# Optimization experiments

Measured on AMD Instinct MI355X. Metric: run time of the kernel, lower is better.

## Reference

```python
import jax, jax.numpy as jnp
import numpy as np

H = 4096; NH = 32; HD = 128; SCALE = HD ** -0.5
PREFILLS = [1024, 512, 768, 256]; DOFF = sum(PREFILLS)
DEC = 32; LMAX = 512; T = DOFF + DEC
NLORA = 4; RANK = 16
SEG = [0, 648, 1296, 1944, 2592]  # static lora segment offsets (cumsum of lens)
NEG = -1e30


def _rope_tables(pos):
    # pos: int array [...]; returns cos/sin of shape [..., HD]
    inv = 1.0 / (10000.0 ** (jnp.arange(0, HD, 2, dtype=jnp.float32) / HD))
    freqs = pos.astype(jnp.float32)[..., None] * inv
    emb = jnp.concatenate([freqs, freqs], axis=-1)
    return jnp.cos(emb), jnp.sin(emb)


def _apply_rope(x, cos, sin):
    # x: [..., HD]; cos/sin broadcastable to x
    x1, x2 = x[..., :HD // 2], x[..., HD // 2:]
    return x * cos + jnp.concatenate([-x2, x1], axis=-1) * sin


def _add_lora(y, x, wa, wb):
    # Punica add_lora: per-segment y += (x @ wa[i]) @ wb[i], segments static
    for i in range(NLORA):
        s, e = SEG[i], SEG[i + 1]
        y = y.at[s:e].add((x[s:e] @ wa[i]) @ wb[i])
    return y


def setup_inputs() -> dict:
    key = jax.random.key(0)
    ks = jax.random.split(key, 16)
    sc = np.float32(1.0 / np.sqrt(H))
    lsc = np.float32(1.0 / np.sqrt(H))
    inp = {
        "hidden_states": jax.random.normal(ks[0], (T, H), jnp.float32),
        "wq": jax.random.normal(ks[1], (H, H), jnp.float32) * sc,
        "wk": jax.random.normal(ks[2], (H, H), jnp.float32) * sc,
        "wv": jax.random.normal(ks[3], (H, H), jnp.float32) * sc,
        "wo": jax.random.normal(ks[4], (H, H), jnp.float32) * sc,
        "la_q": jax.random.normal(ks[5], (NLORA, H, RANK), jnp.float32) * lsc,
        "lb_q": jax.random.normal(ks[6], (NLORA, RANK, H), jnp.float32) * lsc,
        "la_k": jax.random.normal(ks[7], (NLORA, H, RANK), jnp.float32) * lsc,
        "lb_k": jax.random.normal(ks[8], (NLORA, RANK, H), jnp.float32) * lsc,
        "la_v": jax.random.normal(ks[9], (NLORA, H, RANK), jnp.float32) * lsc,
        "lb_v": jax.random.normal(ks[10], (NLORA, RANK, H), jnp.float32) * lsc,
        "la_o": jax.random.normal(ks[11], (NLORA, H, RANK), jnp.float32) * lsc,
        "lb_o": jax.random.normal(ks[12], (NLORA, RANK, H), jnp.float32) * lsc,
        "k_cache": jax.random.normal(ks[13], (DEC, LMAX, NH, HD), jnp.float32),
        "v_cache": jax.random.normal(ks[14], (DEC, LMAX, NH, HD), jnp.float32),
        "kv_lens": jax.random.randint(ks[15], (DEC,), 0, 450, jnp.int32),
    }
    return inp


def reference(hidden_states, wq, wk, wv, wo, la_q, lb_q, la_k, lb_k,
              la_v, lb_v, la_o, lb_o, k_cache, v_cache, kv_lens):
    # fused QKV + segmented batched LoRA
    q = _add_lora(hidden_states @ wq, hidden_states, la_q, lb_q)
    k = _add_lora(hidden_states @ wk, hidden_states, la_k, lb_k)
    v = _add_lora(hidden_states @ wv, hidden_states, la_v, lb_v)

    outs = []
    # ragged prefill: per-request causal attention with inline rotary (beg=0)
    off = 0
    for s_len in PREFILLS:
        qi = q[off:off + s_len].reshape(s_len, NH, HD)
        ki = k[off:off + s_len].reshape(s_len, NH, HD)
        vi = v[off:off + s_len].reshape(s_len, NH, HD)
        cos, sin = _rope_tables(jnp.arange(s_len))
        cos, sin = cos[:, None, :], sin[:, None, :]
        qi = _apply_rope(qi, cos, sin)
        ki = _apply_rope(ki, cos, sin)
        scores = jnp.einsum('qhd,khd->hqk', qi, ki) * SCALE
        causal = jnp.tril(jnp.ones((s_len, s_len), bool))
        scores = jnp.where(causal[None], scores, NEG)
        p = jax.nn.softmax(scores, axis=-1)
        outs.append(jnp.einsum('hqk,khd->qhd', p, vi).reshape(s_len, H))
        off += s_len

    # paged/batched decode: append new k/v at kv_lens, rope-on-the-fly attention
    qd = q[DOFF:].reshape(DEC, NH, HD)
    kd = k[DOFF:].reshape(DEC, NH, HD)
    vd = v[DOFF:].reshape(DEC, NH, HD)
    b = jnp.arange(DEC)
    kc = k_cache.at[b, kv_lens].set(kd)
    vc = v_cache.at[b, kv_lens].set(vd)
    cosq, sinq = _rope_tables(kv_lens)            # new token position = kv_len
    qd = _apply_rope(qd, cosq[:, None, :], sinq[:, None, :])
    cosk, sink = _rope_tables(jnp.arange(LMAX))   # cache positions 0..LMAX-1
    kc_r = _apply_rope(kc, cosk[None, :, None, :], sink[None, :, None, :])
    scores = jnp.einsum('bhd,blhd->bhl', qd, kc_r) * SCALE
    valid = jnp.arange(LMAX)[None, :] <= kv_lens[:, None]  # [DEC, LMAX]
    scores = jnp.where(valid[:, None, :], scores, NEG)
    p = jax.nn.softmax(scores, axis=-1)
    outs.append(jnp.einsum('bhl,blhd->bhd', p, vc).reshape(DEC, H))

    attn = jnp.concatenate(outs, axis=0)          # [T, H]
    o = attn @ wo
    o = _add_lora(o, attn, la_o, lb_o)
    return o
```

## Files before the change

### kernel.cpp

```cpp
#include <hip/hip_runtime.h>
#include <hip/hip_bf16.h>


#define H_    4096
#define NH_   32
#define HD_   128
#define T_    2592
#define DOFF_ 2560
#define DEC_  32
#define LMAX_ 512
#define RANK_ 16
#define MPAD_ 2816

__constant__ float SCALE_ = 0.08838834764831845f;

typedef __bf16 bf16x8 __attribute__((ext_vector_type(8)));
typedef __bf16 bf16x4 __attribute__((ext_vector_type(4)));
typedef float  f32x4  __attribute__((ext_vector_type(4)));

__device__ __forceinline__ void async_cp16(const __bf16* g, __bf16* l) {
    __builtin_amdgcn_global_load_lds(
        (const __attribute__((address_space(1))) void*)g,
        (__attribute__((address_space(3))) void*)l, 16, 0, 0);
}

__global__ __launch_bounds__(256)
void prep1_kernel(const float* __restrict__ X, __bf16* __restrict__ Xb,
                  const float* __restrict__ la0, const float* __restrict__ la1,
                  const float* __restrict__ la2, __bf16* __restrict__ TMP16,
                  const float* __restrict__ wq, const float* __restrict__ wk,
                  const float* __restrict__ wv, const float* __restrict__ wo,
                  __bf16* __restrict__ wT, __bf16* __restrict__ woT,
                  const float* __restrict__ lbq, const float* __restrict__ lbk,
                  const float* __restrict__ lbv, const float* __restrict__ lbo,
                  __bf16* __restrict__ WB16, __bf16* __restrict__ WBo16,
                  float* __restrict__ cost, float* __restrict__ sint)
{
    const int bid = blockIdx.x;
    const int tid = threadIdx.x;

    if (bid < T_) {
        const int r = bid;
        const float* xr = X + (size_t)r * H_;
        __bf16* br = Xb + (size_t)r * H_;
        #pragma unroll
        for (int i = 0; i < 4; ++i) {
            float4 v = ((const float4*)xr)[tid + i * 256];
            bf16x4 w; w[0] = (__bf16)v.x; w[1] = (__bf16)v.y; w[2] = (__bf16)v.z; w[3] = (__bf16)v.w;
            ((bf16x4*)br)[tid + i * 256] = w;
        }
        const int si = (r < 648) ? 0 : (r < 1296 ? 1 : (r < 1944 ? 2 : 3));
        const int c    = tid & 15;
        const int part = tid >> 4;
        const float* wa0 = la0 + (size_t)si * H_ * RANK_;
        const float* wa1 = la1 + (size_t)si * H_ * RANK_;
        const float* wa2 = la2 + (size_t)si * H_ * RANK_;
        float s0 = 0.f, s1 = 0.f, s2 = 0.f;
        const int h0 = part * 256;
        for (int h = h0; h < h0 + 256; ++h) {
            const float xv = xr[h];
            s0 += xv * wa0[(size_t)h * RANK_ + c];
            s1 += xv * wa1[(size_t)h * RANK_ + c];
            s2 += xv * wa2[(size_t)h * RANK_ + c];
        }
        __shared__ float red[3][16][17];
        red[0][part][c] = s0; red[1][part][c] = s1; red[2][part][c] = s2;
        __syncthreads();
        if (tid < 192) {
            const int z = tid >> 6, cc = tid & 63;
            float t = 0.f;
            if ((cc >> 4) == si) {
                #pragma unroll
                for (int p = 0; p < 16; ++p) t += red[z][p][cc & 15];
            }
            TMP16[((size_t)z * MPAD_ + r) * 64 + cc] = (__bf16)t;
        }
    } else if (bid < T_ + 16384) {
        const int t = bid - T_;
        const int z = t >> 12;
        const int rem = t & 4095;
        const int bx = (rem >> 6) * 64;
        const int by = (rem & 63) * 64;
        const float* W = (z == 0) ? wq : (z == 1 ? wk : (z == 2 ? wv : wo));
        __bf16* To = (z < 3) ? wT + (size_t)z * H_ * H_ : woT;
        __shared__ float s[64][65];
        #pragma unroll
        for (int i = 0; i < 4; ++i) {
            const int idx = i * 256 + tid;
            const int r  = idx >> 4;
            const int c4 = (idx & 15) * 4;
            float4 v = *(const float4*)&W[(size_t)(by + r) * H_ + bx + c4];
            s[r][c4] = v.x; s[r][c4 + 1] = v.y; s[r][c4 + 2] = v.z; s[r][c4 + 3] = v.w;
        }
        __syncthreads();
        #pragma unroll
        for (int i = 0; i < 2; ++i) {
            const int idx = i * 256 + tid;
            const int n  = idx >> 3;
            const int kc = (idx & 7) * 8;
            bf16x8 w;
            #pragma unroll
            for (int j = 0; j < 8; ++j) w[j] = (__bf16)s[kc + j][n];
            *(bf16x8*)&To[(size_t)(bx + n) * H_ + by + kc] = w;
        }
    } else if (bid < T_ + 16384 + 64) {
        const int t = bid - (T_ + 16384);
        const int z = t >> 4;
        const int n = (t & 15) * 256 + tid;
        const float* lb = (z == 0) ? lbq : (z == 1 ? lbk : (z == 2 ? lbv : lbo));
        __bf16* dst = (z < 3) ? WB16 + ((size_t)z * H_ + n) * 64 : WBo16 + (size_t)n * 64;
        __bf16 row[64];
        #pragma unroll
        for (int si = 0; si < 4; ++si)
            #pragma unroll
            for (int c = 0; c < 16; ++c)
                row[si * 16 + c] = (__bf16)lb[((size_t)si * 16 + c) * H_ + n];
        #pragma unroll
        for (int i = 0; i < 8; ++i) *(bf16x8*)&dst[i * 8] = *(const bf16x8*)&row[i * 8];
    } else {
        const int t = bid - (T_ + 16384 + 64);
        const int p = t * 4 + (tid >> 6);
        const int i = tid & 63;
        const float inv = powf(10000.f, -(float)(2 * i) / (float)HD_);
        const float a = (float)p * inv;
        cost[p * 64 + i] = cosf(a);
        sint[p * 64 + i] = sinf(a);
    }
}

__global__ __launch_bounds__(512, 2)
void gemm_qkv(const __bf16* __restrict__ A, const __bf16* __restrict__ Bt,
              const __bf16* __restrict__ TMP16, const __bf16* __restrict__ WB16,
              __bf16* __restrict__ O0, __bf16* __restrict__ O1, __bf16* __restrict__ O2, int M)
{
    const int hw = blockIdx.y * 21 + blockIdx.x;
    const int work = (hw & 7) * 126 + (hw >> 3);
    const int bm0 = (work % 21) * 128;
    const int bn0 = (work / 21) * 256;

    __shared__ __align__(16) __bf16 Asl[3][128 * 64];
    __shared__ __align__(16) __bf16 Bsl[3][256 * 64];

    const int tid = threadIdx.x, lane = tid & 63, wid = tid >> 6;
    const int wr = wid >> 2, wc = wid & 3;
    const int fr = lane & 15, fq = lane >> 4;

    int arow[2], aoff[2], brow[4], boff[4];
    #pragma unroll
    for (int i = 0; i < 2; ++i) {
        const int ci = i * 512 + tid;
        arow[i] = ci >> 3;
        aoff[i] = ((ci & 7) ^ (arow[i] & 7)) * 8;
    }
    #pragma unroll
    for (int i = 0; i < 4; ++i) {
        const int ci = i * 512 + tid;
        brow[i] = ci >> 3;
        boff[i] = ((ci & 7) ^ (brow[i] & 7)) * 8;
    }
    const __bf16* Ab = A  + (size_t)bm0 * H_;
    const __bf16* Bb = Bt + (size_t)bn0 * H_;

    auto stageA = [&](int buf, int kt2) {
        const int kb = kt2 * 64;
        #pragma unroll
        for (int i = 0; i < 2; ++i)
            async_cp16(Ab + (size_t)arow[i] * H_ + kb + aoff[i],
                       &Asl[buf][(i * 512 + wid * 64) * 8]);
    };
    auto stageB1 = [&](int buf, int kt2) {
        async_cp16(Bb + (size_t)brow[0] * H_ + kt2 * 64 + boff[0],
                   &Bsl[buf][(wid * 64) * 8]);
    };
    auto stageB3 = [&](int buf, int kt2) {
        const int kb = kt2 * 64;
        #pragma unroll
        for (int i = 1; i < 4; ++i)
            async_cp16(Bb + (size_t)brow[i] * H_ + kb + boff[i],
                       &Bsl[buf][(i * 512 + wid * 64) * 8]);
    };
    auto rdA = [&](int buf, int kh, int mi) -> bf16x8 {
        const int row = wr * 64 + mi * 16 + fr;
        const int pc  = (kh * 4 + fq) ^ (row & 7);
        return *(const bf16x8*)&Asl[buf][row * 64 + pc * 8];
    };
    auto rdB = [&](int buf, int kh, int nj) -> bf16x8 {
        const int row = wc * 64 + nj * 16 + fr;
        const int pc  = (kh * 4 + fq) ^ (row & 7);
        return *(const bf16x8*)&Bsl[buf][row * 64 + pc * 8];
    };

    f32x4 acc[4][4] = {};

    stageA(0, 0); stageB1(0, 0); stageB3(0, 0);
    stageA(1, 1); stageB1(1, 1); stageB3(1, 1);
    asm volatile("s_waitcnt vmcnt(6)");
    __builtin_amdgcn_sched_barrier(0);
    __builtin_amdgcn_s_barrier();

    const int NT = H_ / 64;
    int cur = 0, nxt = 2;
    for (int kt = 0; kt < NT; ++kt) {
        const bool pf = (kt + 2 < NT);
        bf16x8 af[4], bfr[4];

        #pragma unroll
        for (int mi = 0; mi < 4; ++mi) af[mi] = rdA(cur, 0, mi);
        #pragma unroll
        for (int nj = 0; nj < 4; ++nj) bfr[nj] = rdB(cur, 0, nj);
        if (pf) { stageA(nxt, kt + 2); stageB1(nxt, kt + 2); }
        __builtin_amdgcn_s_barrier();
        asm volatile("s_waitcnt lgkmcnt(0)");
        __builtin_amdgcn_sched_barrier(0);
        __builtin_amdgcn_s_setprio(1);
        #pragma unroll
        for (int mi = 0; mi < 4; ++mi)
            #pragma unroll
            for (int nj = 0; nj < 4; ++nj)
                acc[mi][nj] = __builtin_amdgcn_mfma_f32_16x16x32_bf16(af[mi], bfr[nj], acc[mi][nj], 0, 0, 0);
        __builtin_amdgcn_s_setprio(0);
        __builtin_amdgcn_s_barrier();

        #pragma unroll
        for (int mi = 0; mi < 4; ++mi) af[mi] = rdA(cur, 1, mi);
        #pragma unroll
        for (int nj = 0; nj < 4; ++nj) bfr[nj] = rdB(cur, 1, nj);
        if (pf) stageB3(nxt, kt + 2);
        __builtin_amdgcn_s_barrier();
        asm volatile("s_waitcnt lgkmcnt(0)");
        __builtin_amdgcn_sched_barrier(0);
        __builtin_amdgcn_s_setprio(1);
        #pragma unroll
        for (int mi = 0; mi < 4; ++mi)
            #pragma unroll
            for (int nj = 0; nj < 4; ++nj)
                acc[mi][nj] = __builtin_amdgcn_mfma_f32_16x16x32_bf16(af[mi], bfr[nj], acc[mi][nj], 0, 0, 0);
        __builtin_amdgcn_s_setprio(0);
        if (pf)               asm volatile("s_waitcnt vmcnt(6)");
        else if (kt + 1 < NT) asm volatile("s_waitcnt vmcnt(0)");
        __builtin_amdgcn_sched_barrier(0);
        __builtin_amdgcn_s_barrier();

        cur = (cur == 2) ? 0 : cur + 1;
        nxt = (nxt == 2) ? 0 : nxt + 1;
    }

    const int colbase = bn0 + wc * 64;
    const int mat = colbase >> 12;
    __bf16* O = (mat == 0) ? O0 : (mat == 1 ? O1 : O2);
    const __bf16* TPm = TMP16 + (size_t)mat * MPAD_ * 64;
    bf16x8 aT[4][2], bW[4][2];
    #pragma unroll
    for (int mi = 0; mi < 4; ++mi)
        #pragma unroll
        for (int kh = 0; kh < 2; ++kh)
            aT[mi][kh] = *(const bf16x8*)&TPm[(size_t)(bm0 + wr * 64 + mi * 16 + fr) * 64 + kh * 32 + fq * 8];
    #pragma unroll
    for (int nj = 0; nj < 4; ++nj)
        #pragma unroll
        for (int kh = 0; kh < 2; ++kh)
            bW[nj][kh] = *(const bf16x8*)&WB16[(size_t)(colbase + nj * 16 + fr) * 64 + kh * 32 + fq * 8];
    #pragma unroll
    for (int mi = 0; mi < 4; ++mi)
        #pragma unroll
        for (int nj = 0; nj < 4; ++nj) {
            acc[mi][nj] = __builtin_amdgcn_mfma_f32_16x16x32_bf16(aT[mi][0], bW[nj][0], acc[mi][nj], 0, 0, 0);
            acc[mi][nj] = __builtin_amdgcn_mfma_f32_16x16x32_bf16(aT[mi][1], bW[nj][1], acc[mi][nj], 0, 0, 0);
        }
    #pragma unroll
    for (int mi = 0; mi < 4; ++mi)
        #pragma unroll
        for (int nj = 0; nj < 4; ++nj) {
            const int cc = (colbase + nj * 16 + fr) & 4095;
            #pragma unroll
            for (int rr = 0; rr < 4; ++rr) {
                const int row = bm0 + wr * 64 + mi * 16 + fq * 4 + rr;
                if (row < M) O[(size_t)row * H_ + cc] = (__bf16)acc[mi][nj][rr];
            }
        }
}

__global__ __launch_bounds__(512, 2)
void gemm_out(const __bf16* __restrict__ A, const __bf16* __restrict__ Bt,
              const __bf16* __restrict__ TMPo16, const __bf16* __restrict__ WBo16,
              float* __restrict__ C, int M, int Ntot)
{
    const int NY = gridDim.y;
    const int total = gridDim.x * NY;
    const int bid = blockIdx.x * NY + blockIdx.y;
    const int q = total >> 3, r8 = total & 7;
    const int xcd = bid & 7, j = bid >> 3;
    const int swz = (xcd < r8 ? xcd * (q + 1) : r8 * (q + 1) + (xcd - r8) * q) + j;
    const int bm0 = (swz / NY) * 256;
    const int bn0 = (swz % NY) * 192;

    __shared__ __align__(16) __bf16 Asl[2][256 * 64];
    __shared__ __align__(16) __bf16 Bsl[2][192 * 64];

    const int tid = threadIdx.x, lane = tid & 63, wid = tid >> 6;
    const int wr = wid >> 2, wc = wid & 3;
    const int fr = lane & 15, fq = lane >> 4;

    int arow[4], aoff[4], brow[3], boff[3];
    #pragma unroll
    for (int i = 0; i < 4; ++i) {
        const int ci = i * 512 + tid;
        arow[i] = ci >> 3;
        aoff[i] = ((ci & 7) ^ (arow[i] & 7)) * 8;
    }
    #pragma unroll
    for (int i = 0; i < 3; ++i) {
        const int ci = i * 512 + tid;
        brow[i] = ci >> 3;
        boff[i] = ((ci & 7) ^ (brow[i] & 7)) * 8;
    }
    const __bf16* Ab = A  + (size_t)bm0 * H_;
    const __bf16* Bb = Bt + (size_t)bn0 * H_;

    auto stage = [&](int buf, int kt1) {
        const int kb = kt1 * 64;
        #pragma unroll
        for (int i = 0; i < 4; ++i)
            async_cp16(Ab + (size_t)arow[i] * H_ + kb + aoff[i],
                       &Asl[buf][(i * 512 + wid * 64) * 8]);
        #pragma unroll
        for (int i = 0; i < 3; ++i)
            async_cp16(Bb + (size_t)brow[i] * H_ + kb + boff[i],
                       &Bsl[buf][(i * 512 + wid * 64) * 8]);
    };
    auto rdA = [&](int buf, int kh, int mi) -> bf16x8 {
        const int row = wr * 128 + mi * 16 + fr;
        const int kc  = kh * 4 + fq;
        return *(const bf16x8*)&Asl[buf][row * 64 + ((kc ^ (row & 7)) << 3)];
    };
    auto rdB = [&](int buf, int kh, int nj) -> bf16x8 {
        const int row = wc * 48 + nj * 16 + fr;
        const int kc  = kh * 4 + fq;
        return *(const bf16x8*)&Bsl[buf][row * 64 + ((kc ^ (row & 7)) << 3)];
    };

    f32x4 acc[8][3] = {};

    stage(0, 0);
    asm volatile("s_waitcnt vmcnt(0)");
    __builtin_amdgcn_sched_barrier(0);
    __builtin_amdgcn_s_barrier();

    const int NT = H_ / 64;
    for (int kt = 0; kt < NT; ++kt) {
        const int cur = kt & 1, nb = cur ^ 1;
        const bool pf = (kt + 1 < NT);
        bf16x8 af[8], bfr[3];

        #pragma unroll
        for (int mi = 0; mi < 8; ++mi) af[mi] = rdA(cur, 0, mi);
        #pragma unroll
        for (int nj = 0; nj < 3; ++nj) bfr[nj] = rdB(cur, 0, nj);
        if (pf) stage(nb, kt + 1);
        __builtin_amdgcn_s_barrier();
        asm volatile("s_waitcnt lgkmcnt(0)");
        __builtin_amdgcn_sched_barrier(0);
        __builtin_amdgcn_s_setprio(1);
        #pragma unroll
        for (int mi = 0; mi < 8; ++mi)
            #pragma unroll
            for (int nj = 0; nj < 3; ++nj)
                acc[mi][nj] = __builtin_amdgcn_mfma_f32_16x16x32_bf16(af[mi], bfr[nj], acc[mi][nj], 0, 0, 0);
        __builtin_amdgcn_s_setprio(0);
        __builtin_amdgcn_s_barrier();

        #pragma unroll
        for (int mi = 0; mi < 8; ++mi) af[mi] = rdA(cur, 1, mi);
        #pragma unroll
        for (int nj = 0; nj < 3; ++nj) bfr[nj] = rdB(cur, 1, nj);
        __builtin_amdgcn_s_barrier();
        asm volatile("s_waitcnt lgkmcnt(0)");
        __builtin_amdgcn_sched_barrier(0);
        __builtin_amdgcn_s_setprio(1);
        #pragma unroll
        for (int mi = 0; mi < 8; ++mi)
            #pragma unroll
            for (int nj = 0; nj < 3; ++nj)
                acc[mi][nj] = __builtin_amdgcn_mfma_f32_16x16x32_bf16(af[mi], bfr[nj], acc[mi][nj], 0, 0, 0);
        __builtin_amdgcn_s_setprio(0);
        asm volatile("s_waitcnt vmcnt(0)");
        __builtin_amdgcn_sched_barrier(0);
        __builtin_amdgcn_s_barrier();
    }

    const int colw = bn0 + wc * 48;
    bf16x8 aT[8][2], bW[3][2];
    #pragma unroll
    for (int mi = 0; mi < 8; ++mi)
        #pragma unroll
        for (int kh = 0; kh < 2; ++kh)
            aT[mi][kh] = *(const bf16x8*)&TMPo16[(size_t)(bm0 + wr * 128 + mi * 16 + fr) * 64 + kh * 32 + fq * 8];
    #pragma unroll
    for (int nj = 0; nj < 3; ++nj)
        #pragma unroll
        for (int kh = 0; kh < 2; ++kh)
            bW[nj][kh] = *(const bf16x8*)&WBo16[(size_t)(colw + nj * 16 + fr) * 64 + kh * 32 + fq * 8];
    #pragma unroll
    for (int mi = 0; mi < 8; ++mi)
        #pragma unroll
        for (int nj = 0; nj < 3; ++nj) {
            acc[mi][nj] = __builtin_amdgcn_mfma_f32_16x16x32_bf16(aT[mi][0], bW[nj][0], acc[mi][nj], 0, 0, 0);
            acc[mi][nj] = __builtin_amdgcn_mfma_f32_16x16x32_bf16(aT[mi][1], bW[nj][1], acc[mi][nj], 0, 0, 0);
        }
    #pragma unroll
    for (int mi = 0; mi < 8; ++mi)
        #pragma unroll
        for (int nj = 0; nj < 3; ++nj) {
            const int col = colw + nj * 16 + fr;
            if (col < Ntot) {
                #pragma unroll
                for (int rr = 0; rr < 4; ++rr) {
                    const int row = bm0 + wr * 128 + mi * 16 + fq * 4 + rr;
                    if (row < M) C[(size_t)row * H_ + col] = acc[mi][nj][rr];
                }
            }
        }
}

__global__ __launch_bounds__(256)
void lora_tmp_bf16_kernel(const __bf16* __restrict__ X,
                          const float* __restrict__ la, __bf16* __restrict__ TMPo16)
{
    const int r = blockIdx.x;
    const int si = (r < 648) ? 0 : (r < 1296 ? 1 : (r < 1944 ? 2 : 3));
    const float* wa = la + (size_t)si * H_ * RANK_;
    const int c    = threadIdx.x & 15;
    const int part = threadIdx.x >> 4;
    const __bf16* xr = X + (size_t)r * H_;
    float s = 0.f;
    const int h0 = part * 256;
    for (int h = h0; h < h0 + 256; ++h) s += (float)xr[h] * wa[(size_t)h * RANK_ + c];
    __shared__ float red[16][17];
    red[part][c] = s;
    __syncthreads();
    if (threadIdx.x < 64) {
        const int cc = threadIdx.x;
        float t = 0.f;
        if ((cc >> 4) == si) {
            #pragma unroll
            for (int p = 0; p < 16; ++p) t += red[p][cc & 15];
        }
        TMPo16[(size_t)r * 64 + cc] = (__bf16)t;
    }
}

__global__ __launch_bounds__(256)
void post1_kernel(__bf16* __restrict__ q16, __bf16* __restrict__ k16,
                  const __bf16* __restrict__ v16, __bf16* __restrict__ vT,
                  const int* __restrict__ kv_lens,
                  const float* __restrict__ cost, const float* __restrict__ sint)
{
    const int bid = blockIdx.x;
    const int tid = threadIdx.x;

    if (bid < T_) {
        const int r = bid;
        int pos; bool dok;
        if (r < DOFF_) {
            if      (r < 1024) pos = r;
            else if (r < 1536) pos = r - 1024;
            else if (r < 2304) pos = r - 1536;
            else               pos = r - 2304;
            dok = true;
        } else {
            pos = kv_lens[r - DOFF_];
            dok = false;
        }
        const int h = tid >> 3, sub = tid & 7;
        const int i0 = sub * 8;
        const size_t b1 = (size_t)r * H_ + h * HD_ + i0;
        const size_t b2 = b1 + 64;

        float cs[8], sn[8];
        #pragma unroll
        for (int j = 0; j < 8; ++j) { cs[j] = cost[pos * 64 + i0 + j]; sn[j] = sint[pos * 64 + i0 + j]; }

        {
            bf16x8 x1 = *(const bf16x8*)&q16[b1], x2 = *(const bf16x8*)&q16[b2];
            bf16x8 o1, o2;
            #pragma unroll
            for (int j = 0; j < 8; ++j) {
                const float f1 = (float)x1[j], f2 = (float)x2[j];
                o1[j] = (__bf16)(f1 * cs[j] - f2 * sn[j]);
                o2[j] = (__bf16)(f2 * cs[j] + f1 * sn[j]);
            }
            *(bf16x8*)&q16[b1] = o1; *(bf16x8*)&q16[b2] = o2;
        }
        if (dok) {
            bf16x8 x1 = *(const bf16x8*)&k16[b1], x2 = *(const bf16x8*)&k16[b2];
            bf16x8 o1, o2;
            #pragma unroll
            for (int j = 0; j < 8; ++j) {
                const float f1 = (float)x1[j], f2 = (float)x2[j];
                o1[j] = (__bf16)(f1 * cs[j] - f2 * sn[j]);
                o2[j] = (__bf16)(f2 * cs[j] + f1 * sn[j]);
            }
            *(bf16x8*)&k16[b1] = o1; *(bf16x8*)&k16[b2] = o2;
        }
    } else {
        const int t = bid - T_;
        const int tb = t % 40;
        const int h  = t / 40;
        __shared__ __bf16 s[64][136];
        #pragma unroll
        for (int i = 0; i < 4; ++i) {
            const int idx = i * 256 + tid;
            const int row = idx >> 4;
            const int c8  = (idx & 15) * 8;
            *(bf16x8*)&s[row][c8] = *(const bf16x8*)&v16[(size_t)(tb * 64 + row) * H_ + h * HD_ + c8];
        }
        __syncthreads();
        #pragma unroll
        for (int i = 0; i < 4; ++i) {
            const int idx = i * 256 + tid;
            const int d = idx >> 3;
            const int c = idx & 7;
            bf16x8 w;
            #pragma unroll
            for (int j = 0; j < 8; ++j) w[j] = s[c * 8 + j][d];
            *(bf16x8*)&vT[(size_t)(h * HD_ + d) * T_ + tb * 64 + c * 8] = w;
        }
    }
}

__global__ __launch_bounds__(256)
void attn_kernel(const __bf16* __restrict__ q16, const __bf16* __restrict__ k16,
                 const __bf16* __restrict__ v16, const __bf16* __restrict__ vT,
                 const float* __restrict__ kc, const float* __restrict__ vc,
                 const int* __restrict__ kv_lens,
                 const float* __restrict__ cost, const float* __restrict__ sint,
                 __bf16* __restrict__ attn16)
{
    const int h = blockIdx.y;
    const int tid = threadIdx.x, lane = tid & 63, wid = tid >> 6;

    if (blockIdx.x < 40) {
        const int qb = blockIdx.x;
        int soff, qoff;
        if      (qb < 16) { soff = 0;    qoff = qb * 64; }
        else if (qb < 24) { soff = 1024; qoff = (qb - 16) * 64; }
        else if (qb < 36) { soff = 1536; qoff = (qb - 24) * 64; }
        else              { soff = 2304; qoff = (qb - 36) * 64; }

        __shared__ __align__(16) __bf16 Kl[2][64 * 128];
        __shared__ __align__(16) __bf16 Vl[2][128 * 64];
        __shared__ __align__(16) __bf16 Pl[4][16 * 64];

        const int fr = lane & 15, fq = lane >> 4;
        const int grow0 = soff + qoff + wid * 16;
        bf16x8 qf[4];
        #pragma unroll
        for (int ks = 0; ks < 4; ++ks)
            qf[ks] = *(const bf16x8*)&q16[(size_t)(grow0 + fr) * H_ + h * HD_ + ks * 32 + fq * 8];

        auto stageK = [&](int buf, int t) {
            const int kt = t * 64;
            #pragma unroll
            for (int i = 0; i < 4; ++i) {
                const int chunk = i * 256 + tid;
                const int row = chunk >> 4, c = chunk & 15;
                async_cp16(k16 + (size_t)(soff + kt + row) * H_ + h * HD_ + ((c ^ (row & 7)) * 8),
                           Kl[buf] + (size_t)(i * 256 + wid * 64) * 8);
            }
        };
        auto stageV = [&](int buf, int t) {
            const int kt = t * 64;
            #pragma unroll
            for (int i = 0; i < 4; ++i) {
                const int chunk = i * 256 + tid;
                const int row = chunk >> 3, c = chunk & 7;
                async_cp16(vT + (size_t)(h * HD_ + row) * T_ + soff + kt + ((c ^ (row & 7)) * 8),
                           Vl[buf] + (size_t)(i * 256 + wid * 64) * 8);
            }
        };

        float m[4], l[4];
        #pragma unroll
        for (int r = 0; r < 4; ++r) { m[r] = -1e30f; l[r] = 0.f; }
        f32x4 o[8] = {};

        const int ntiles = qoff / 64 + 1;
        stageK(0, 0); stageV(0, 0);
        if (ntiles > 1) {
            stageK(1, 1); stageV(1, 1);
            asm volatile("s_waitcnt vmcnt(8)");
        } else {
            asm volatile("s_waitcnt vmcnt(0)");
        }
        __builtin_amdgcn_sched_barrier(0);
        __builtin_amdgcn_s_barrier();

        for (int t = 0; t < ntiles; ++t) {
            const int b = t & 1;
            const int kt = t * 64;

            f32x4 s[4] = {};
            __builtin_amdgcn_s_setprio(1);
            #pragma unroll
            for (int sub = 0; sub < 4; ++sub)
                #pragma unroll
                for (int ks = 0; ks < 4; ++ks) {
                    bf16x8 bk = *(const bf16x8*)&Kl[b][(sub * 16 + fr) * 128 + (((ks * 4 + fq) ^ (fr & 7)) * 8)];
                    s[sub] = __builtin_amdgcn_mfma_f32_16x16x32_bf16(qf[ks], bk, s[sub], 0, 0, 0);
                }
            __builtin_amdgcn_s_setprio(0);

            float p[4][4];
            #pragma unroll
            for (int sub = 0; sub < 4; ++sub)
                #pragma unroll
                for (int r = 0; r < 4; ++r) {
                    const int qpos = qoff + wid * 16 + fq * 4 + r;
                    const int kpos = kt + sub * 16 + fr;
                    p[sub][r] = (kpos <= qpos) ? s[sub][r] * SCALE_ : -1e30f;
                }
            float tm2[4];
            #pragma unroll
            for (int r = 0; r < 4; ++r) {
                float tm = fmaxf(fmaxf(p[0][r], p[1][r]), fmaxf(p[2][r], p[3][r]));
                tm = fmaxf(tm, __shfl_xor(tm, 1));
                tm = fmaxf(tm, __shfl_xor(tm, 2));
                tm = fmaxf(tm, __shfl_xor(tm, 4));
                tm = fmaxf(tm, __shfl_xor(tm, 8));
                tm2[r] = tm;
            }
            bool need = false;
            #pragma unroll
            for (int r = 0; r < 4; ++r) need |= (tm2[r] > m[r] + 8.f);
            if (__any(need)) {
                #pragma unroll
                for (int r = 0; r < 4; ++r) {
                    const float mn = fmaxf(m[r], tm2[r]);
                    const float f  = __expf(m[r] - mn);
                    m[r] = mn;
                    l[r] *= f;
                    #pragma unroll
                    for (int c = 0; c < 8; ++c) o[c][r] *= f;
                }
            }
            #pragma unroll
            for (int r = 0; r < 4; ++r) {
                float ls = 0.f;
                #pragma unroll
                for (int sub = 0; sub < 4; ++sub) {
                    p[sub][r] = __expf(p[sub][r] - m[r]);
                    ls += p[sub][r];
                }
                l[r] += ls;
            }

            #pragma unroll
            for (int sub = 0; sub < 4; ++sub)
                #pragma unroll
                for (int r = 0; r < 4; ++r) {
                    const int qr = fq * 4 + r;
                    Pl[wid][qr * 64 + ((sub * 16 + fr) ^ ((qr & 7) << 3))] = (__bf16)p[sub][r];
                }
            bf16x8 pa[2];
            #pragma unroll
            for (int a = 0; a < 2; ++a)
                pa[a] = *(const bf16x8*)&Pl[wid][fr * 64 + (((a * 4 + fq) ^ (fr & 7)) * 8)];

            __builtin_amdgcn_s_setprio(1);
            #pragma unroll
            for (int a = 0; a < 2; ++a)
                #pragma unroll
                for (int c = 0; c < 8; ++c) {
                    bf16x8 bv = *(const bf16x8*)&Vl[b][(c * 16 + fr) * 64 + (((a * 4 + fq) ^ (fr & 7)) * 8)];
                    o[c] = __builtin_amdgcn_mfma_f32_16x16x32_bf16(pa[a], bv, o[c], 0, 0, 0);
                }
            __builtin_amdgcn_s_setprio(0);

            __builtin_amdgcn_s_barrier();
            __builtin_amdgcn_sched_barrier(0);
            if (t + 2 < ntiles) { stageK(b, t + 2); stageV(b, t + 2); }
            if (t + 1 < ntiles) {
                if (t + 2 < ntiles) asm volatile("s_waitcnt vmcnt(8)");
                else                asm volatile("s_waitcnt vmcnt(0)");
                __builtin_amdgcn_sched_barrier(0);
                __builtin_amdgcn_s_barrier();
            }
        }

        float inv[4];
        #pragma unroll
        for (int r = 0; r < 4; ++r) {
            float ls = l[r];
            ls += __shfl_xor(ls, 1); ls += __shfl_xor(ls, 2);
            ls += __shfl_xor(ls, 4); ls += __shfl_xor(ls, 8);
            inv[r] = 1.f / ls;
        }
        #pragma unroll
        for (int c = 0; c < 8; ++c)
            #pragma unroll
            for (int r = 0; r < 4; ++r)
                attn16[(size_t)(grow0 + fq * 4 + r) * H_ + h * HD_ + c * 16 + fr] = (__bf16)(o[c][r] * inv[r]);
    } else {
        const int b = blockIdx.x - 40;
        const int kvlen = kv_lens[b];
        const int L = kvlen + 1;
        const int w = wid;

        __shared__ float sc_s[LMAX_];
        __shared__ float red[4];
        __shared__ float oacc[HD_];

        const __bf16* qrow = q16 + (size_t)(DOFF_ + b) * H_ + h * HD_;
        const float q1 = (float)qrow[lane], q2 = (float)qrow[lane + 64];
        const __bf16* kdrow = k16 + (size_t)(DOFF_ + b) * H_ + h * HD_;

        for (int l = w; l < L; l += 4) {
            float k1, k2;
            if (l == kvlen) { k1 = (float)kdrow[lane]; k2 = (float)kdrow[lane + 64]; }
            else {
                const float* src = kc + (((size_t)b * LMAX_ + l) * NH_ + h) * HD_;
                k1 = src[lane]; k2 = src[lane + 64];
            }
            const float c = cost[l * 64 + lane], s = sint[l * 64 + lane];
            float d = q1 * (k1 * c - k2 * s) + q2 * (k2 * c + k1 * s);
            #pragma unroll
            for (int off = 1; off < 64; off <<= 1) d += __shfl_xor(d, off);
            if (lane == 0) sc_s[l] = d * SCALE_;
        }
        __syncthreads();

        float mx = -1e30f;
        for (int i = tid; i < L; i += 256) mx = fmaxf(mx, sc_s[i]);
        #pragma unroll
        for (int off = 1; off < 64; off <<= 1) mx = fmaxf(mx, __shfl_xor(mx, off));
        if (lane == 0) red[w] = mx;
        __syncthreads();
        mx = fmaxf(fmaxf(red[0], red[1]), fmaxf(red[2], red[3]));
        __syncthreads();

        float sum = 0.f;
        for (int i = tid; i < L; i += 256) { const float e = __expf(sc_s[i] - mx); sc_s[i] = e; sum += e; }
        #pragma unroll
        for (int off = 1; off < 64; off <<= 1) sum += __shfl_xor(sum, off);
        if (lane == 0) red[w] = sum;
        __syncthreads();
        sum = red[0] + red[1] + red[2] + red[3];
        const float inv = 1.f / sum;

        const int d = tid & 127, team = tid >> 7;
        const __bf16* vdrow = v16 + (size_t)(DOFF_ + b) * H_ + h * HD_;
        float acc = 0.f;
        for (int l = team; l < L; l += 2) {
            float vv;
            if (l == kvlen) vv = (float)vdrow[d];
            else            vv = vc[(((size_t)b * LMAX_ + l) * NH_ + h) * HD_ + d];
            acc += sc_s[l] * vv;
        }
        if (team == 1) oacc[d] = acc;
        __syncthreads();
        if (team == 0) attn16[(size_t)(DOFF_ + b) * H_ + h * HD_ + d] = (__bf16)((acc + oacc[d]) * inv);
    }
}

extern "C" void kernel_launch(void* const* d_in, const int* in_sizes, int n_in,
                              void* d_out, int out_size, void* d_ws, size_t ws_size,
                              hipStream_t stream)
{
    const float* hs     = (const float*)d_in[0];
    const float* wq     = (const float*)d_in[1];
    const float* wk     = (const float*)d_in[2];
    const float* wv     = (const float*)d_in[3];
    const float* wo     = (const float*)d_in[4];
    const float* la_q   = (const float*)d_in[5];
    const float* lb_q   = (const float*)d_in[6];
    const float* la_k   = (const float*)d_in[7];
    const float* lb_k   = (const float*)d_in[8];
    const float* la_v   = (const float*)d_in[9];
    const float* lb_v   = (const float*)d_in[10];
    const float* la_o   = (const float*)d_in[11];
    const float* lb_o   = (const float*)d_in[12];
    const float* kcache = (const float*)d_in[13];
    const float* vcache = (const float*)d_in[14];
    const int*   kvlen  = (const int*)d_in[15];
    float* out = (float*)d_out;

    float*  costab = (float*)d_ws;
    float*  sintab = costab + 1024 * 64;
    __bf16* TMP16  = (__bf16*)(sintab + 1024 * 64);
    __bf16* TMPo16 = TMP16 + (size_t)3 * MPAD_ * 64;
    __bf16* WB16   = TMPo16 + (size_t)MPAD_ * 64;
    __bf16* WBo16  = WB16 + (size_t)3 * H_ * 64;
    __bf16* q16    = WBo16 + (size_t)4352 * 64;
    __bf16* k16    = q16 + (size_t)T_ * H_;
    __bf16* v16    = k16 + (size_t)T_ * H_;
    __bf16* hsb    = v16 + (size_t)T_ * H_;
    __bf16* wT     = hsb + (size_t)MPAD_ * H_;
    __bf16* woT    = wT + (size_t)3 * H_ * H_;
    __bf16* vT     = woT + (size_t)H_ * H_;
    __bf16* attn16 = hsb;

    prep1_kernel<<<dim3(T_ + 16384 + 64 + 256), dim3(256), 0, stream>>>(
        hs, hsb, la_q, la_k, la_v, TMP16,
        wq, wk, wv, wo, wT, woT,
        lb_q, lb_k, lb_v, lb_o, WB16, WBo16, costab, sintab);
    gemm_qkv<<<dim3(21, 48), dim3(512), 0, stream>>>(
        hsb, wT, TMP16, WB16, q16, k16, v16, T_);
    post1_kernel<<<dim3(T_ + 1280), dim3(256), 0, stream>>>(
        q16, k16, v16, vT, kvlen, costab, sintab);
    attn_kernel<<<dim3(72, 32), dim3(256), 0, stream>>>(
        q16, k16, v16, vT, kcache, vcache, kvlen, costab, sintab, attn16);
    lora_tmp_bf16_kernel<<<dim3(T_), dim3(256), 0, stream>>>(attn16, la_o, TMPo16);
    gemm_out<<<dim3(11, 22), dim3(512), 0, stream>>>(
        attn16, woT, TMPo16, WBo16, out, T_, H_);
}
```

Measured before the change: 1.088 ms.

## Split attention into per-wave prefill kernel and separate decode kernel

```diff
diff --git a/kernel.cpp b/kernel.cpp
--- a/kernel.cpp
+++ b/kernel.cpp
@@ -529,237 +529,191 @@
 }
 
 __global__ __launch_bounds__(256)
-void attn_kernel(const __bf16* __restrict__ q16, const __bf16* __restrict__ k16,
-                 const __bf16* __restrict__ v16, const __bf16* __restrict__ vT,
-                 const float* __restrict__ kc, const float* __restrict__ vc,
-                 const int* __restrict__ kv_lens,
-                 const float* __restrict__ cost, const float* __restrict__ sint,
-                 __bf16* __restrict__ attn16)
+void prefill_attn_wave(const __bf16* __restrict__ q16, const __bf16* __restrict__ k16,
+                       const __bf16* __restrict__ vT, __bf16* __restrict__ attn16)
 {
-    const int h = blockIdx.y;
     const int tid = threadIdx.x, lane = tid & 63, wid = tid >> 6;
-
-    if (blockIdx.x < 40) {
-        const int qb = blockIdx.x;
-        int soff, qoff;
-        if      (qb < 16) { soff = 0;    qoff = qb * 64; }
-        else if (qb < 24) { soff = 1024; qoff = (qb - 16) * 64; }
-        else if (qb < 36) { soff = 1536; qoff = (qb - 24) * 64; }
-        else              { soff = 2304; qoff = (qb - 36) * 64; }
-
-        __shared__ __align__(16) __bf16 Kl[2][64 * 128];
-        __shared__ __align__(16) __bf16 Vl[2][128 * 64];
-        __shared__ __align__(16) __bf16 Pl[4][16 * 64];
-
-        const int fr = lane & 15, fq = lane >> 4;
-        const int grow0 = soff + qoff + wid * 16;
-        bf16x8 qf[4];
-        #pragma unroll
-        for (int ks = 0; ks < 4; ++ks)
-            qf[ks] = *(const bf16x8*)&q16[(size_t)(grow0 + fr) * H_ + h * HD_ + ks * 32 + fq * 8];
-
-        auto stageK = [&](int buf, int t) {
-            const int kt = t * 64;
-            #pragma unroll
-            for (int i = 0; i < 4; ++i) {
-                const int chunk = i * 256 + tid;
-                const int row = chunk >> 4, c = chunk & 15;
-                async_cp16(k16 + (size_t)(soff + kt + row) * H_ + h * HD_ + ((c ^ (row & 7)) * 8),
-                           Kl[buf] + (size_t)(i * 256 + wid * 64) * 8);
-            }
-        };
-        auto stageV = [&](int buf, int t) {
-            const int kt = t * 64;
-            #pragma unroll
-            for (int i = 0; i < 4; ++i) {
-                const int chunk = i * 256 + tid;
-                const int row = chunk >> 3, c = chunk & 7;
-                async_cp16(vT + (size_t)(h * HD_ + row) * T_ + soff + kt + ((c ^ (row & 7)) * 8),
-                           Vl[buf] + (size_t)(i * 256 + wid * 64) * 8);
-            }
-        };
-
-        float m[4], l[4];
-        #pragma unroll
-        for (int r = 0; r < 4; ++r) { m[r] = -1e30f; l[r] = 0.f; }
-        f32x4 o[8] = {};
-
-        const int ntiles = qoff / 64 + 1;
-        stageK(0, 0); stageV(0, 0);
-        if (ntiles > 1) {
-            stageK(1, 1); stageV(1, 1);
-            asm volatile("s_waitcnt vmcnt(8)");
-        } else {
-            asm volatile("s_waitcnt vmcnt(0)");
-        }
-        __builtin_amdgcn_sched_barrier(0);
-        __builtin_amdgcn_s_barrier();
-
-        for (int t = 0; t < ntiles; ++t) {
-            const int b = t & 1;
-            const int kt = t * 64;
-
-            f32x4 s[4] = {};
-            __builtin_amdgcn_s_setprio(1);
-            #pragma unroll
-            for (int sub = 0; sub < 4; ++sub)
+    const int h = blockIdx.x / 40;
+    const int g = (blockIdx.x % 40) * 4 + wid;
+    int soff, gq;
+    if      (g < 64)  { soff = 0;    gq = g; }
+    else if (g < 96)  { soff = 1024; gq = g - 64; }
+    else if (g < 144) { soff = 1536; gq = g - 96; }
+    else              { soff = 2304; gq = g - 144; }
+    const int qoff = gq * 16;
+    const int fr = lane & 15, fq = lane >> 4;
+
+    __shared__ __align__(16) __bf16 Pl[4][16 * 32];
+    __bf16* Plw = Pl[wid];
+
+    const int grow0 = soff + qoff;
+    bf16x8 qf[4];
+    #pragma unroll
+    for (int ks = 0; ks < 4; ++ks)
+        qf[ks] = *(const bf16x8*)&q16[(size_t)(grow0 + fr) * H_ + h * HD_ + ks * 32 + fq * 8];
+
+    float m[4], l[4];
+    #pragma unroll
+    for (int r = 0; r < 4; ++r) { m[r] = -1e30f; l[r] = 0.f; }
+    f32x4 o[8] = {};
+
+    const int ntiles = (qoff + 15) / 32 + 1;
+    const __bf16* Kb = k16 + h * HD_;
+    const __bf16* Vb = vT + (size_t)h * HD_ * T_;
+
+    for (int t = 0; t < ntiles; ++t) {
+        const int kt = t * 32;
+
+        f32x4 s[2] = {};
+        #pragma unroll
+        for (int sub = 0; sub < 2; ++sub)
+            #pragma unroll
+            for (int ks = 0; ks < 4; ++ks) {
+                bf16x8 bk = *(const bf16x8*)&Kb[(size_t)(soff + kt + sub * 16 + fr) * H_ + ks * 32 + fq * 8];
+                s[sub] = __builtin_amdgcn_mfma_f32_16x16x32_bf16(qf[ks], bk, s[sub], 0, 0, 0);
+            }
+
+        float p[2][4];
+        #pragma unroll
+        for (int sub = 0; sub < 2; ++sub)
+            #pragma unroll
+            for (int r = 0; r < 4; ++r) {
+                const int qpos = qoff + fq * 4 + r;
+                const int kpos = kt + sub * 16 + fr;
+                p[sub][r] = (kpos <= qpos) ? s[sub][r] * SCALE_ : -1e30f;
+            }
+        float tm2[4];
+        #pragma unroll
+        for (int r = 0; r < 4; ++r) {
+            float tm = fmaxf(p[0][r], p[1][r]);
+            tm = fmaxf(tm, __shfl_xor(tm, 1));
+            tm = fmaxf(tm, __shfl_xor(tm, 2));
+            tm = fmaxf(tm, __shfl_xor(tm, 4));
+            tm = fmaxf(tm, __shfl_xor(tm, 8));
+            tm2[r] = tm;
+        }
+        bool need = false;
+        #pragma unroll
+        for (int r = 0; r < 4; ++r) need |= (tm2[r] > m[r] + 8.f);
+        if (__any(need)) {
+            #pragma unroll
+            for (int r = 0; r < 4; ++r) {
+                const float mn = fmaxf(m[r], tm2[r]);
+                const float f  = __expf(m[r] - mn);
+                m[r] = mn;
+                l[r] *= f;
                 #pragma unroll
-                for (int ks = 0; ks < 4; ++ks) {
-                    bf16x8 bk = *(const bf16x8*)&Kl[b][(sub * 16 + fr) * 128 + (((ks * 4 + fq) ^ (fr & 7)) * 8)];
-                    s[sub] = __builtin_amdgcn_mfma_f32_16x16x32_bf16(qf[ks], bk, s[sub], 0, 0, 0);
-                }
-            __builtin_amdgcn_s_setprio(0);
-
-            float p[4][4];
-            #pragma unroll
-            for (int sub = 0; sub < 4; ++sub)
-                #pragma unroll
-                for (int r = 0; r < 4; ++r) {
-                    const int qpos = qoff + wid * 16 + fq * 4 + r;
-                    const int kpos = kt + sub * 16 + fr;
-                    p[sub][r] = (kpos <= qpos) ? s[sub][r] * SCALE_ : -1e30f;
-                }
-            float tm2[4];
+                for (int c = 0; c < 8; ++c) o[c][r] *= f;
+            }
+        }
+        #pragma unroll
+        for (int r = 0; r < 4; ++r) {
+            float ls = 0.f;
+            #pragma unroll
+            for (int sub = 0; sub < 2; ++sub) {
+                p[sub][r] = __expf(p[sub][r] - m[r]);
+                ls += p[sub][r];
+            }
+            l[r] += ls;
+        }
+
+        #pragma unroll
+        for (int sub = 0; sub < 2; ++sub)
             #pragma unroll
             for (int r = 0; r < 4; ++r) {
-                float tm = fmaxf(fmaxf(p[0][r], p[1][r]), fmaxf(p[2][r], p[3][r]));
-                tm = fmaxf(tm, __shfl_xor(tm, 1));
-                tm = fmaxf(tm, __shfl_xor(tm, 2));
-                tm = fmaxf(tm, __shfl_xor(tm, 4));
-                tm = fmaxf(tm, __shfl_xor(tm, 8));
-                tm2[r] = tm;
-            }
-            bool need = false;
-            #pragma unroll
-            for (int r = 0; r < 4; ++r) need |= (tm2[r] > m[r] + 8.f);
-            if (__any(need)) {
-                #pragma unroll
-                for (int r = 0; r < 4; ++r) {
-                    const float mn = fmaxf(m[r], tm2[r]);
-                    const float f  = __expf(m[r] - mn);
-                    m[r] = mn;
-                    l[r] *= f;
-                    #pragma unroll
-                    for (int c = 0; c < 8; ++c) o[c][r] *= f;
-                }
-            }
-            #pragma unroll
-            for (int r = 0; r < 4; ++r) {
-                float ls = 0.f;
-                #pragma unroll
-                for (int sub = 0; sub < 4; ++sub) {
-                    p[sub][r] = __expf(p[sub][r] - m[r]);
-                    ls += p[sub][r];
-                }
-                l[r] += ls;
-            }
-
-            #pragma unroll
-            for (int sub = 0; sub < 4; ++sub)
-                #pragma unroll
-                for (int r = 0; r < 4; ++r) {
-                    const int qr = fq * 4 + r;
-                    Pl[wid][qr * 64 + ((sub * 16 + fr) ^ ((qr & 7) << 3))] = (__bf16)p[sub][r];
-                }
-            bf16x8 pa[2];
-            #pragma unroll
-            for (int a = 0; a < 2; ++a)
-                pa[a] = *(const bf16x8*)&Pl[wid][fr * 64 + (((a * 4 + fq) ^ (fr & 7)) * 8)];
-
-            __builtin_amdgcn_s_setprio(1);
-            #pragma unroll
-            for (int a = 0; a < 2; ++a)
-                #pragma unroll
-                for (int c = 0; c < 8; ++c) {
-                    bf16x8 bv = *(const bf16x8*)&Vl[b][(c * 16 + fr) * 64 + (((a * 4 + fq) ^ (fr & 7)) * 8)];
-                    o[c] = __builtin_amdgcn_mfma_f32_16x16x32_bf16(pa[a], bv, o[c], 0, 0, 0);
-                }
-            __builtin_amdgcn_s_setprio(0);
-
-            __builtin_amdgcn_s_barrier();
-            __builtin_amdgcn_sched_barrier(0);
-            if (t + 2 < ntiles) { stageK(b, t + 2); stageV(b, t + 2); }
-            if (t + 1 < ntiles) {
-                if (t + 2 < ntiles) asm volatile("s_waitcnt vmcnt(8)");
-                else                asm volatile("s_waitcnt vmcnt(0)");
-                __builtin_amdgcn_sched_barrier(0);
-                __builtin_amdgcn_s_barrier();
-            }
-        }
-
-        float inv[4];
-        #pragma unroll
-        for (int r = 0; r < 4; ++r) {
-            float ls = l[r];
-            ls += __shfl_xor(ls, 1); ls += __shfl_xor(ls, 2);
-            ls += __shfl_xor(ls, 4); ls += __shfl_xor(ls, 8);
-            inv[r] = 1.f / ls;
-        }
-        #pragma unroll
-        for (int c = 0; c < 8; ++c)
-            #pragma unroll
-            for (int r = 0; r < 4; ++r)
-                attn16[(size_t)(grow0 + fq * 4 + r) * H_ + h * HD_ + c * 16 + fr] = (__bf16)(o[c][r] * inv[r]);
-    } else {
-        const int b = blockIdx.x - 40;
-        const int kvlen = kv_lens[b];
-        const int L = kvlen + 1;
-        const int w = wid;
-
-        __shared__ float sc_s[LMAX_];
-        __shared__ float red[4];
-        __shared__ float oacc[HD_];
-
-        const __bf16* qrow = q16 + (size_t)(DOFF_ + b) * H_ + h * HD_;
-        const float q1 = (float)qrow[lane], q2 = (float)qrow[lane + 64];
-        const __bf16* kdrow = k16 + (size_t)(DOFF_ + b) * H_ + h * HD_;
-
-        for (int l = w; l < L; l += 4) {
-            float k1, k2;
-            if (l == kvlen) { k1 = (float)kdrow[lane]; k2 = (float)kdrow[lane + 64]; }
-            else {
-                const float* src = kc + (((size_t)b * LMAX_ + l) * NH_ + h) * HD_;
-                k1 = src[lane]; k2 = src[lane + 64];
-            }
-            const float c = cost[l * 64 + lane], s = sint[l * 64 + lane];
-            float d = q1 * (k1 * c - k2 * s) + q2 * (k2 * c + k1 * s);
-            #pragma unroll
-            for (int off = 1; off < 64; off <<= 1) d += __shfl_xor(d, off);
-            if (lane == 0) sc_s[l] = d * SCALE_;
-        }
-        __syncthreads();
-
-        float mx = -1e30f;
-        for (int i = tid; i < L; i += 256) mx = fmaxf(mx, sc_s[i]);
-        #pragma unroll
-        for (int off = 1; off < 64; off <<= 1) mx = fmaxf(mx, __shfl_xor(mx, off));
-        if (lane == 0) red[w] = mx;
-        __syncthreads();
-        mx = fmaxf(fmaxf(red[0], red[1]), fmaxf(red[2], red[3]));
-        __syncthreads();
-
-        float sum = 0.f;
-        for (int i = tid; i < L; i += 256) { const float e = __expf(sc_s[i] - mx); sc_s[i] = e; sum += e; }
-        #pragma unroll
-        for (int off = 1; off < 64; off <<= 1) sum += __shfl_xor(sum, off);
-        if (lane == 0) red[w] = sum;
-        __syncthreads();
-        sum = red[0] + red[1] + red[2] + red[3];
-        const float inv = 1.f / sum;
-
-        const int d = tid & 127, team = tid >> 7;
-        const __bf16* vdrow = v16 + (size_t)(DOFF_ + b) * H_ + h * HD_;
-        float acc = 0.f;
-        for (int l = team; l < L; l += 2) {
-            float vv;
-            if (l == kvlen) vv = (float)vdrow[d];
-            else            vv = vc[(((size_t)b * LMAX_ + l) * NH_ + h) * HD_ + d];
-            acc += sc_s[l] * vv;
-        }
-        if (team == 1) oacc[d] = acc;
-        __syncthreads();
-        if (team == 0) attn16[(size_t)(DOFF_ + b) * H_ + h * HD_ + d] = (__bf16)((acc + oacc[d]) * inv);
-    }
+                const int qr = fq * 4 + r;
+                const int col = sub * 16 + fr;
+                Plw[qr * 32 + ((((col >> 3) ^ (qr & 3)) & 3) * 8) + (col & 7)] = (__bf16)p[sub][r];
+            }
+        bf16x8 pa = *(const bf16x8*)&Plw[fr * 32 + (((fq ^ (fr & 3)) & 3) * 8)];
+
+        #pragma unroll
+        for (int c = 0; c < 8; ++c) {
+            bf16x8 bv = *(const bf16x8*)&Vb[(size_t)(c * 16 + fr) * T_ + soff + kt + fq * 8];
+            o[c] = __builtin_amdgcn_mfma_f32_16x16x32_bf16(pa, bv, o[c], 0, 0, 0);
+        }
+    }
+
+    float inv[4];
+    #pragma unroll
+    for (int r = 0; r < 4; ++r) {
+        float ls = l[r];
+        ls += __shfl_xor(ls, 1); ls += __shfl_xor(ls, 2);
+        ls += __shfl_xor(ls, 4); ls += __shfl_xor(ls, 8);
+        inv[r] = 1.f / ls;
+    }
+    #pragma unroll
+    for (int c = 0; c < 8; ++c)
+        #pragma unroll
+        for (int r = 0; r < 4; ++r)
+            attn16[(size_t)(grow0 + fq * 4 + r) * H_ + h * HD_ + c * 16 + fr] = (__bf16)(o[c][r] * inv[r]);
+}
+
+__global__ __launch_bounds__(256)
+void decode_attn_kernel(const __bf16* __restrict__ q16, const __bf16* __restrict__ k16,
+                        const __bf16* __restrict__ v16, const float* __restrict__ kc,
+                        const float* __restrict__ vc, const int* __restrict__ kv_lens,
+                        const float* __restrict__ cost, const float* __restrict__ sint,
+                        __bf16* __restrict__ attn16)
+{
+    const int b = blockIdx.x, h = blockIdx.y;
+    const int kvlen = kv_lens[b];
+    const int L = kvlen + 1;
+    const int tid = threadIdx.x, lane = tid & 63, w = tid >> 6;
+
+    __shared__ float sc_s[LMAX_];
+    __shared__ float red[4];
+    __shared__ float oacc[HD_];
+
+    const __bf16* qrow = q16 + (size_t)(DOFF_ + b) * H_ + h * HD_;
+    const float q1 = (float)qrow[lane], q2 = (float)qrow[lane + 64];
+    const __bf16* kdrow = k16 + (size_t)(DOFF_ + b) * H_ + h * HD_;
+
+    for (int l = w; l < L; l += 4) {
+        float k1, k2;
+        if (l == kvlen) { k1 = (float)kdrow[lane]; k2 = (float)kdrow[lane + 64]; }
+        else {
+            const float* src = kc + (((size_t)b * LMAX_ + l) * NH_ + h) * HD_;
+            k1 = src[lane]; k2 = src[lane + 64];
+        }
+        const float c = cost[l * 64 + lane], s = sint[l * 64 + lane];
+        float d = q1 * (k1 * c - k2 * s) + q2 * (k2 * c + k1 * s);
+        #pragma unroll
+        for (int off = 1; off < 64; off <<= 1) d += __shfl_xor(d, off);
+        if (lane == 0) sc_s[l] = d * SCALE_;
+    }
+    __syncthreads();
+
+    float mx = -1e30f;
+    for (int i = tid; i < L; i += 256) mx = fmaxf(mx, sc_s[i]);
+    #pragma unroll
+    for (int off = 1; off < 64; off <<= 1) mx = fmaxf(mx, __shfl_xor(mx, off));
+    if (lane == 0) red[w] = mx;
+    __syncthreads();
+    mx = fmaxf(fmaxf(red[0], red[1]), fmaxf(red[2], red[3]));
+    __syncthreads();
+
+    float sum = 0.f;
+    for (int i = tid; i < L; i += 256) { const float e = __expf(sc_s[i] - mx); sc_s[i] = e; sum += e; }
+    #pragma unroll
+    for (int off = 1; off < 64; off <<= 1) sum += __shfl_xor(sum, off);
+    if (lane == 0) red[w] = sum;
+    __syncthreads();
+    sum = red[0] + red[1] + red[2] + red[3];
+    const float inv = 1.f / sum;
+
+    const int d = tid & 127, team = tid >> 7;
+    const __bf16* vdrow = v16 + (size_t)(DOFF_ + b) * H_ + h * HD_;
+    float acc = 0.f;
+    for (int l = team; l < L; l += 2) {
+        float vv;
+        if (l == kvlen) vv = (float)vdrow[d];
+        else            vv = vc[(((size_t)b * LMAX_ + l) * NH_ + h) * HD_ + d];
+        acc += sc_s[l] * vv;
+    }
+    if (team == 1) oacc[d] = acc;
+    __syncthreads();
+    if (team == 0) attn16[(size_t)(DOFF_ + b) * H_ + h * HD_ + d] = (__bf16)((acc + oacc[d]) * inv);
 }
 
 extern "C" void kernel_launch(void* const* d_in, const int* in_sizes, int n_in,
@@ -807,8 +761,9 @@
         hsb, wT, TMP16, WB16, q16, k16, v16, T_);
     post1_kernel<<<dim3(T_ + 1280), dim3(256), 0, stream>>>(
         q16, k16, v16, vT, kvlen, costab, sintab);
-    attn_kernel<<<dim3(72, 32), dim3(256), 0, stream>>>(
-        q16, k16, v16, vT, kcache, vcache, kvlen, costab, sintab, attn16);
+    prefill_attn_wave<<<dim3(1280), dim3(256), 0, stream>>>(q16, k16, vT, attn16);
+    decode_attn_kernel<<<dim3(DEC_, NH_), dim3(256), 0, stream>>>(q16, k16, v16, kcache, vcache,
+                                                                  kvlen, costab, sintab, attn16);
     lora_tmp_bf16_kernel<<<dim3(T_), dim3(256), 0, stream>>>(attn16, la_o, TMPo16);
     gemm_out<<<dim3(11, 22), dim3(512), 0, stream>>>(
         attn16, woT, TMPo16, WBo16, out, T_, H_);
```

Measured after the change: 1.077 ms. About the same (-1.0%).
